# Optimization experiments

Hardware: AMD Instinct MI355X
Metric: run time of the kernel (lower is better)

## Reference

```python
import jax, jax.numpy as jnp
import numpy as np

B, T, H, W, C = 8, 32, 64, 64, 3
F = 24        # conv filters
U = 128       # lstm units
O = 1         # output units

def _conv(x, w, b):
    # x: [N,H,W,Cin], w: [3,3,Cin,Cout], SAME padding, linear activation
    y = jax.lax.conv_general_dilated(x, w, window_strides=(1, 1), padding='SAME',
                                     dimension_numbers=('NHWC', 'HWIO', 'NHWC'))
    return y + b

def setup_inputs() -> dict:
    key = jax.random.key(0)
    ks = jax.random.split(key, 16)
    s = lambda *shape: 0.05
    inp = {
        'x': jax.random.normal(ks[0], (B, T, H, W, C), dtype=jnp.float32),
        'conv1_w': jax.random.normal(ks[1], (3, 3, C, F), dtype=jnp.float32) * 0.1,
        'conv1_b': jnp.zeros((F,), jnp.float32),
        'conv2_w': jax.random.normal(ks[2], (3, 3, F, F), dtype=jnp.float32) * 0.1,
        'conv2_b': jnp.zeros((F,), jnp.float32),
        'Wf': jax.random.normal(ks[3], (F + U, U), dtype=jnp.float32) * 0.08,
        'bf': jnp.zeros((U,), jnp.float32),
        'Wi': jax.random.normal(ks[4], (F + U, U), dtype=jnp.float32) * 0.08,
        'bi': jnp.zeros((U,), jnp.float32),
        'Wc': jax.random.normal(ks[5], (F + U, U), dtype=jnp.float32) * 0.08,
        'bc': jnp.zeros((U,), jnp.float32),
        'Wo': jax.random.normal(ks[6], (F + U, U), dtype=jnp.float32) * 0.08,
        'bo': jnp.zeros((U,), jnp.float32),
        'out_w': jax.random.normal(ks[7], (U, O), dtype=jnp.float32) * 0.08,
        'out_b': jnp.zeros((O,), jnp.float32),
    }
    return inp

def reference(x, conv1_w, conv1_b, conv2_w, conv2_b, Wf, bf, Wi, bi, Wc, bc, Wo, bo, out_w, out_b):
    b, t, h, w, c = x.shape
    # CNN block (per-frame): two linear 3x3 convs, no pooling inside block
    xr = x.reshape(b * t, h, w, c)
    xr = _conv(xr, conv1_w, conv1_b)
    xr = _conv(xr, conv2_w, conv2_b)
    # TimeDistributed(GlobalAvgPool2D): mean over H,W -> [B,T,F]
    feat = xr.reshape(b, t, h, w, -1).mean(axis=(2, 3))

    # custom LSTM recurrence over time via scan
    def step(carry, xt):
        hs, cs = carry
        z = jnp.concatenate([xt, hs], axis=-1)           # [B, F+U]
        f = jax.nn.sigmoid(z @ Wf + bf)
        i = jax.nn.sigmoid(z @ Wi + bi)
        g = jnp.tanh(z @ Wc + bc)
        o = jax.nn.sigmoid(z @ Wo + bo)
        c_new = cs * f + i * g
        h_new = jnp.tanh(c_new) * o
        return (h_new, c_new), h_new

    h0 = jnp.zeros((b, Wf.shape[1]), x.dtype)
    c0 = jnp.zeros((b, Wf.shape[1]), x.dtype)
    _, hs = jax.lax.scan(step, (h0, c0), jnp.swapaxes(feat, 0, 1))  # [T,B,U]
    hs = jnp.swapaxes(hs, 0, 1)                                     # [B,T,U]
    return hs @ out_w + out_b                                       # [B,T,O]
```

## Files before the change

### kernel.cpp

```cpp
#include <hip/hip_runtime.h>
#include <math.h>

#define Bb 8
#define Tt 32
#define Hh 64
#define Ww 64
#define Cc 3
#define Ff 24
#define Uu 128

__global__ void convfeat_kernel(const float* __restrict__ x,
                                const float* __restrict__ w1, const float* __restrict__ b1,
                                const float* __restrict__ w2, const float* __restrict__ b2,
                                float* __restrict__ feat) {
    int n = blockIdx.x;
    const float* xf = x + (size_t)n * (Hh * Ww * Cc);
    int tid  = threadIdx.x;
    int row  = tid >> 2;
    int part = tid & 3;

    __shared__ float partial[256][3];
    __shared__ float rowsum[64][3];
    __shared__ float colv[64][12];
    __shared__ float st[75];
    __shared__ float yst[24][9];

    float s0 = 0.f, s1 = 0.f, s2 = 0.f;
    const float4* p4 = (const float4*)(xf + (row * Ww + part * 16) * Cc);
#pragma unroll
    for (int i = 0; i < 12; ++i) {
        float4 v = p4[i];
        int j = i * 4;
        float vv[4] = {v.x, v.y, v.z, v.w};
#pragma unroll
        for (int l = 0; l < 4; ++l) {
            int c = (j + l) % 3;
            if (c == 0) s0 += vv[l]; else if (c == 1) s1 += vv[l]; else s2 += vv[l];
        }
    }
    partial[tid][0] = s0; partial[tid][1] = s1; partial[tid][2] = s2;

    if (tid < 64) {
        int r = tid;
#pragma unroll
        for (int w4 = 0; w4 < 4; ++w4) {
            int w = (w4 < 2) ? w4 : 60 + w4;
#pragma unroll
            for (int c = 0; c < 3; ++c) colv[r][w4 * 3 + c] = xf[(r * Ww + w) * Cc + c];
        }
    }
    __syncthreads();

    if (part == 0) {
#pragma unroll
        for (int c = 0; c < 3; ++c)
            rowsum[row][c] = partial[tid][c] + partial[tid + 1][c]
                           + partial[tid + 2][c] + partial[tid + 3][c];
    }
    __syncthreads();

    if (tid < 3) {
        float t = 0.f;
        for (int r = 0; r < 64; ++r) t += rowsum[r][tid];
        st[tid * 25 + 0] = t;
    }
    if (tid >= 4 && tid < 16) {
        int k = tid - 4; int ri = k / 3, c = k % 3;
        int r = (ri < 2) ? ri : 60 + ri;
        st[c * 25 + 1 + ri] = rowsum[r][c];
    }
    if (tid >= 64 && tid < 76) {
        int k = tid - 64;
        float t = 0.f;
        for (int r = 0; r < 64; ++r) t += colv[r][k];
        int wi = k / 3, c = k % 3;
        st[c * 25 + 5 + wi] = t;
    }
    if (tid >= 128 && tid < 176) {
        int k = tid - 128; int pos = k / 3, c = k % 3;
        int ri = pos >> 2, wi = pos & 3;
        int r = (ri < 2) ? ri : 60 + ri;
        int w = (wi < 2) ? wi : 60 + wi;
        st[c * 25 + 9 + pos] = xf[(r * Ww + w) * Cc + c];
    }
    __syncthreads();

    if (tid < 24) {
        int f = tid;
        float Sy = 0, r0 = 0, r63 = 0, c0 = 0, c63 = 0, y00 = 0, y0W = 0, yH0 = 0, yHW = 0;
        for (int c = 0; c < 3; ++c) {
            const float* S = st + c * 25;
            float Sx = S[0];
            float rX[4] = {S[1], S[2], S[3], S[4]};
            float cX[4] = {S[5], S[6], S[7], S[8]};
            const float* X = S + 9;
            #define W1(p, q) w1[(((p) * 3 + (q)) * 3 + c) * 24 + f]
#pragma unroll
            for (int p = 0; p < 3; ++p)
#pragma unroll
                for (int q = 0; q < 3; ++q) {
                    float t = Sx;
                    if (p == 0) t -= rX[3];
                    if (p == 2) t -= rX[0];
                    if (q == 0) t -= cX[3];
                    if (q == 2) t -= cX[0];
                    if (p == 0 && q == 0) t += X[3 * 4 + 3];
                    if (p == 0 && q == 2) t += X[3 * 4 + 0];
                    if (p == 2 && q == 0) t += X[0 * 4 + 3];
                    if (p == 2 && q == 2) t += X[0 * 4 + 0];
                    Sy += W1(p, q) * t;
                }
#pragma unroll
            for (int q = 0; q < 3; ++q) {
                float Rr0  = rX[0] - ((q == 0) ? X[0 * 4 + 3] : 0.f) - ((q == 2) ? X[0 * 4 + 0] : 0.f);
                float Rr1  = rX[1] - ((q == 0) ? X[1 * 4 + 3] : 0.f) - ((q == 2) ? X[1 * 4 + 0] : 0.f);
                float Rr62 = rX[2] - ((q == 0) ? X[2 * 4 + 3] : 0.f) - ((q == 2) ? X[2 * 4 + 0] : 0.f);
                float Rr63 = rX[3] - ((q == 0) ? X[3 * 4 + 3] : 0.f) - ((q == 2) ? X[3 * 4 + 0] : 0.f);
                r0  += W1(1, q) * Rr0  + W1(2, q) * Rr1;
                r63 += W1(0, q) * Rr62 + W1(1, q) * Rr63;
            }
#pragma unroll
            for (int p = 0; p < 3; ++p) {
                float Rc0  = cX[0] - ((p == 0) ? X[3 * 4 + 0] : 0.f) - ((p == 2) ? X[0 * 4 + 0] : 0.f);
                float Rc1  = cX[1] - ((p == 0) ? X[3 * 4 + 1] : 0.f) - ((p == 2) ? X[0 * 4 + 1] : 0.f);
                float Rc62 = cX[2] - ((p == 0) ? X[3 * 4 + 2] : 0.f) - ((p == 2) ? X[0 * 4 + 2] : 0.f);
                float Rc63 = cX[3] - ((p == 0) ? X[3 * 4 + 3] : 0.f) - ((p == 2) ? X[0 * 4 + 3] : 0.f);
                c0  += W1(p, 1) * Rc0  + W1(p, 2) * Rc1;
                c63 += W1(p, 0) * Rc62 + W1(p, 1) * Rc63;
            }
            y00 += W1(1, 1) * X[0 * 4 + 0] + W1(1, 2) * X[0 * 4 + 1]
                 + W1(2, 1) * X[1 * 4 + 0] + W1(2, 2) * X[1 * 4 + 1];
            y0W += W1(1, 0) * X[0 * 4 + 2] + W1(1, 1) * X[0 * 4 + 3]
                 + W1(2, 0) * X[1 * 4 + 2] + W1(2, 1) * X[1 * 4 + 3];
            yH0 += W1(0, 1) * X[2 * 4 + 0] + W1(0, 2) * X[2 * 4 + 1]
                 + W1(1, 1) * X[3 * 4 + 0] + W1(1, 2) * X[3 * 4 + 1];
            yHW += W1(0, 0) * X[2 * 4 + 2] + W1(0, 1) * X[2 * 4 + 3]
                 + W1(1, 0) * X[3 * 4 + 2] + W1(1, 1) * X[3 * 4 + 3];
            #undef W1
        }
        float bb = b1[f];
        yst[f][0] = Sy + 4096.f * bb;
        yst[f][1] = r0 + 64.f * bb;
        yst[f][2] = r63 + 64.f * bb;
        yst[f][3] = c0 + 64.f * bb;
        yst[f][4] = c63 + 64.f * bb;
        yst[f][5] = y00 + bb; yst[f][6] = y0W + bb;
        yst[f][7] = yH0 + bb; yst[f][8] = yHW + bb;
    }
    __syncthreads();

    if (tid < 24) {
        int g = tid;
        float acc = 0.f;
        for (int f = 0; f < 24; ++f) {
            float Sy = yst[f][0], rY0 = yst[f][1], rY63 = yst[f][2], cY0 = yst[f][3], cY63 = yst[f][4];
            float yc00 = yst[f][5], yc0W = yst[f][6], ycH0 = yst[f][7], ycHW = yst[f][8];
#pragma unroll
            for (int p = 0; p < 3; ++p)
#pragma unroll
                for (int q = 0; q < 3; ++q) {
                    float t = Sy;
                    if (p == 0) t -= rY63;
                    if (p == 2) t -= rY0;
                    if (q == 0) t -= cY63;
                    if (q == 2) t -= cY0;
                    if (p == 0 && q == 0) t += ycHW;
                    if (p == 0 && q == 2) t += ycH0;
                    if (p == 2 && q == 0) t += yc0W;
                    if (p == 2 && q == 2) t += yc00;
                    acc += w2[(((p * 3 + q) * 24 + f) * 24) + g] * t;
                }
        }
        feat[(size_t)n * 24 + g] = b2[g] + acc * (1.f / 4096.f);
    }
}

__global__ void gpre_kernel(const float* __restrict__ feat,
                            const float* __restrict__ Wf, const float* __restrict__ bf,
                            const float* __restrict__ Wi, const float* __restrict__ bi,
                            const float* __restrict__ Wc, const float* __restrict__ bc,
                            const float* __restrict__ Wo, const float* __restrict__ bo,
                            float* __restrict__ G) {
    int blk = blockIdx.x;
    int t = blk >> 3, b = blk & 7;
    int tid = threadIdx.x;
    int g = tid >> 7, u = tid & 127;
    const float* W    = (g == 0) ? Wf : (g == 1) ? Wi : (g == 2) ? Wc : Wo;
    const float* bias = (g == 0) ? bf : (g == 1) ? bi : (g == 2) ? bc : bo;
    int n = b * Tt + t;
    float acc = bias[u];
#pragma unroll
    for (int k = 0; k < Ff; ++k) acc += feat[(size_t)n * Ff + k] * W[k * Uu + u];
    G[(size_t)blk * 512 + tid] = acc;
}

__global__ __launch_bounds__(512, 1) void lstm_kernel(
        const float* __restrict__ G,
        const float* __restrict__ Wf, const float* __restrict__ Wi,
        const float* __restrict__ Wc, const float* __restrict__ Wo,
        const float* __restrict__ out_w, const float* __restrict__ out_b,
        float* __restrict__ out) {
    int b = blockIdx.x;
    int tid = threadIdx.x;
    int u = tid & 127;
    int q = tid >> 7;

    float wreg[32][4];
    {
        const float* W0 = Wf + (size_t)(Ff + q * 32) * Uu + u;
        const float* W1 = Wi + (size_t)(Ff + q * 32) * Uu + u;
        const float* W2 = Wc + (size_t)(Ff + q * 32) * Uu + u;
        const float* W3 = Wo + (size_t)(Ff + q * 32) * Uu + u;
#pragma unroll
        for (int j = 0; j < 32; ++j) {
            wreg[j][0] = W0[j * Uu];
            wreg[j][1] = W1[j * Uu];
            wreg[j][2] = W2[j * Uu];
            wreg[j][3] = W3[j * Uu];
        }
    }

    __shared__ float hs[Uu];
    __shared__ float part[4][4][Uu];
    __shared__ float act[4][Uu];
    __shared__ float hist[Tt][Uu];

    float cs = 0.f;
    if (tid < Uu) hs[tid] = 0.f;
    __syncthreads();

    for (int t = 0; t < Tt; ++t) {
        float gx = G[((size_t)(t * Bb + b)) * 512 + tid];

        float p0 = 0.f, p1 = 0.f, p2 = 0.f, p3 = 0.f;
        const float4* h4 = (const float4*)(hs + q * 32);
#pragma unroll
        for (int j4 = 0; j4 < 8; ++j4) {
            float4 hv = h4[j4];
            p0 += wreg[j4 * 4 + 0][0] * hv.x; p1 += wreg[j4 * 4 + 0][1] * hv.x;
            p2 += wreg[j4 * 4 + 0][2] * hv.x; p3 += wreg[j4 * 4 + 0][3] * hv.x;
            p0 += wreg[j4 * 4 + 1][0] * hv.y; p1 += wreg[j4 * 4 + 1][1] * hv.y;
            p2 += wreg[j4 * 4 + 1][2] * hv.y; p3 += wreg[j4 * 4 + 1][3] * hv.y;
            p0 += wreg[j4 * 4 + 2][0] * hv.z; p1 += wreg[j4 * 4 + 2][1] * hv.z;
            p2 += wreg[j4 * 4 + 2][2] * hv.z; p3 += wreg[j4 * 4 + 2][3] * hv.z;
            p0 += wreg[j4 * 4 + 3][0] * hv.w; p1 += wreg[j4 * 4 + 3][1] * hv.w;
            p2 += wreg[j4 * 4 + 3][2] * hv.w; p3 += wreg[j4 * 4 + 3][3] * hv.w;
        }
        part[q][0][u] = p0; part[q][1][u] = p1;
        part[q][2][u] = p2; part[q][3][u] = p3;
        __syncthreads();

        float s = part[0][q][u] + part[1][q][u] + part[2][q][u] + part[3][q][u] + gx;
        float a = (q == 2) ? tanhf(s) : 1.f / (1.f + expf(-s));
        act[q][u] = a;
        __syncthreads();

        if (tid < Uu) {
            float f = act[0][u], i = act[1][u], g = act[2][u], o = act[3][u];
            cs = cs * f + i * g;
            float hn = tanhf(cs) * o;
            hs[u] = hn;
            hist[t][u] = hn;
        }
        __syncthreads();
    }

    int tt = tid >> 4, j = tid & 15;
    const float4* hh = (const float4*)(&hist[tt][j * 8]);
    float4 a0 = hh[0], a1 = hh[1];
    const float* owp = out_w + j * 8;
    float pw = a0.x * owp[0] + a0.y * owp[1] + a0.z * owp[2] + a0.w * owp[3]
             + a1.x * owp[4] + a1.y * owp[5] + a1.z * owp[6] + a1.w * owp[7];
#pragma unroll
    for (int off = 8; off > 0; off >>= 1) pw += __shfl_down(pw, off, 16);
    if (j == 0) out[b * Tt + tt] = pw + out_b[0];
}

extern "C" void kernel_launch(void* const* d_in, const int* in_sizes, int n_in,
                              void* d_out, int out_size, void* d_ws, size_t ws_size,
                              hipStream_t stream) {
    const float* x   = (const float*)d_in[0];
    const float* w1  = (const float*)d_in[1];
    const float* b1  = (const float*)d_in[2];
    const float* w2  = (const float*)d_in[3];
    const float* b2  = (const float*)d_in[4];
    const float* Wf  = (const float*)d_in[5];
    const float* bf  = (const float*)d_in[6];
    const float* Wi  = (const float*)d_in[7];
    const float* bi  = (const float*)d_in[8];
    const float* Wc  = (const float*)d_in[9];
    const float* bc  = (const float*)d_in[10];
    const float* Wo  = (const float*)d_in[11];
    const float* bo  = (const float*)d_in[12];
    const float* ow  = (const float*)d_in[13];
    const float* ob  = (const float*)d_in[14];
    float* out = (float*)d_out;

    float* ws   = (float*)d_ws;
    float* feat = ws;
    float* G    = ws + 6144;

    convfeat_kernel<<<Bb * Tt, 256, 0, stream>>>(x, w1, b1, w2, b2, feat);
    gpre_kernel<<<Bb * Tt, 512, 0, stream>>>(feat, Wf, bf, Wi, bi, Wc, bc, Wo, bo, G);
    lstm_kernel<<<Bb, 512, 0, stream>>>(G, Wf, Wi, Wc, Wo, ow, ob, out);
}
```

Baseline: 42.96 us.

## Fuse input-gate projection into LSTM kernel and use packed FMA with fast activations

Removes the separate gpre kernel launch and its workspace round trip by computing each thread's 24-term input projection inside the LSTM time loop. Each thread now holds the recurrent weights for two units across two gates, so the matmul can use v_pk_fma_f32 inline assembly. Gate partials go to a 16-row shared buffer, and one barrier per step is dropped by doing the activations in the reduction threads. tanh and sigmoid switch to exp2/rcp approximations, which add a little numerical error and leave the activation work serialized in 128 threads.

New measurement: 50.16 us. +16.8%, slower.

```diff
diff --git a/kernel.cpp b/kernel.cpp
--- a/kernel.cpp
+++ b/kernel.cpp
@@ -8,6 +8,17 @@
 #define Cc 3
 #define Ff 24
 #define Uu 128
+
+typedef float v2f __attribute__((ext_vector_type(2)));
+
+__device__ __forceinline__ float fast_sigmoid(float x) {
+    float e = __builtin_amdgcn_exp2f(-1.442695040888963f * x);
+    return __builtin_amdgcn_rcpf(1.f + e);
+}
+__device__ __forceinline__ float fast_tanh(float x) {
+    float e = __builtin_amdgcn_exp2f(-2.885390081777927f * x);
+    return 2.f * __builtin_amdgcn_rcpf(1.f + e) - 1.f;
+}
 
 __global__ void convfeat_kernel(const float* __restrict__ x,
                                 const float* __restrict__ w1, const float* __restrict__ b1,
@@ -175,90 +186,89 @@
     }
 }
 
-__global__ void gpre_kernel(const float* __restrict__ feat,
-                            const float* __restrict__ Wf, const float* __restrict__ bf,
-                            const float* __restrict__ Wi, const float* __restrict__ bi,
-                            const float* __restrict__ Wc, const float* __restrict__ bc,
-                            const float* __restrict__ Wo, const float* __restrict__ bo,
-                            float* __restrict__ G) {
-    int blk = blockIdx.x;
-    int t = blk >> 3, b = blk & 7;
-    int tid = threadIdx.x;
-    int g = tid >> 7, u = tid & 127;
-    const float* W    = (g == 0) ? Wf : (g == 1) ? Wi : (g == 2) ? Wc : Wo;
-    const float* bias = (g == 0) ? bf : (g == 1) ? bi : (g == 2) ? bc : bo;
-    int n = b * Tt + t;
-    float acc = bias[u];
-#pragma unroll
-    for (int k = 0; k < Ff; ++k) acc += feat[(size_t)n * Ff + k] * W[k * Uu + u];
-    G[(size_t)blk * 512 + tid] = acc;
-}
-
 __global__ __launch_bounds__(512, 1) void lstm_kernel(
-        const float* __restrict__ G,
-        const float* __restrict__ Wf, const float* __restrict__ Wi,
-        const float* __restrict__ Wc, const float* __restrict__ Wo,
+        const float* __restrict__ feat,
+        const float* __restrict__ Wf, const float* __restrict__ bf,
+        const float* __restrict__ Wi, const float* __restrict__ bi,
+        const float* __restrict__ Wc, const float* __restrict__ bc,
+        const float* __restrict__ Wo, const float* __restrict__ bo,
         const float* __restrict__ out_w, const float* __restrict__ out_b,
         float* __restrict__ out) {
-    int b = blockIdx.x;
+    int b   = blockIdx.x;
     int tid = threadIdx.x;
-    int u = tid & 127;
-    int q = tid >> 7;
-
-    float wreg[32][4];
-    {
-        const float* W0 = Wf + (size_t)(Ff + q * 32) * Uu + u;
-        const float* W1 = Wi + (size_t)(Ff + q * 32) * Uu + u;
-        const float* W2 = Wc + (size_t)(Ff + q * 32) * Uu + u;
-        const float* W3 = Wo + (size_t)(Ff + q * 32) * Uu + u;
-#pragma unroll
-        for (int j = 0; j < 32; ++j) {
-            wreg[j][0] = W0[j * Uu];
-            wreg[j][1] = W1[j * Uu];
-            wreg[j][2] = W2[j * Uu];
-            wreg[j][3] = W3[j * Uu];
-        }
-    }
+    int up  = tid & 63;
+    int q   = (tid >> 6) & 3;
+    int s   = tid >> 8;
+
+    const float* Wg0 = (s == 0) ? Wf : Wc;
+    const float* Wg1 = (s == 0) ? Wi : Wo;
+
+    v2f w0[32], w1[32];
+#pragma unroll
+    for (int r = 0; r < 32; ++r) {
+        w0[r] = *(const v2f*)(Wg0 + (size_t)(Ff + 32 * q + r) * Uu + 2 * up);
+        w1[r] = *(const v2f*)(Wg1 + (size_t)(Ff + 32 * q + r) * Uu + 2 * up);
+    }
+
+    const float* Wgx = (q & 1) ? Wg1 : Wg0;
+    const float* bgx = (s == 0) ? ((q & 1) ? bi : bf) : ((q & 1) ? bo : bc);
+    int ucol = 2 * up + ((q >> 1) & 1);
+    float w24[Ff];
+#pragma unroll
+    for (int k = 0; k < Ff; ++k) w24[k] = Wgx[(size_t)k * Uu + ucol];
+    float biasv = bgx[ucol];
 
     __shared__ float hs[Uu];
-    __shared__ float part[4][4][Uu];
-    __shared__ float act[4][Uu];
+    __shared__ float part[16][Uu];
     __shared__ float hist[Tt][Uu];
 
     float cs = 0.f;
     if (tid < Uu) hs[tid] = 0.f;
     __syncthreads();
 
+    const float* ftb = feat + (size_t)(b * Tt) * Ff;
+
     for (int t = 0; t < Tt; ++t) {
-        float gx = G[((size_t)(t * Bb + b)) * 512 + tid];
-
-        float p0 = 0.f, p1 = 0.f, p2 = 0.f, p3 = 0.f;
-        const float4* h4 = (const float4*)(hs + q * 32);
-#pragma unroll
-        for (int j4 = 0; j4 < 8; ++j4) {
-            float4 hv = h4[j4];
-            p0 += wreg[j4 * 4 + 0][0] * hv.x; p1 += wreg[j4 * 4 + 0][1] * hv.x;
-            p2 += wreg[j4 * 4 + 0][2] * hv.x; p3 += wreg[j4 * 4 + 0][3] * hv.x;
-            p0 += wreg[j4 * 4 + 1][0] * hv.y; p1 += wreg[j4 * 4 + 1][1] * hv.y;
-            p2 += wreg[j4 * 4 + 1][2] * hv.y; p3 += wreg[j4 * 4 + 1][3] * hv.y;
-            p0 += wreg[j4 * 4 + 2][0] * hv.z; p1 += wreg[j4 * 4 + 2][1] * hv.z;
-            p2 += wreg[j4 * 4 + 2][2] * hv.z; p3 += wreg[j4 * 4 + 2][3] * hv.z;
-            p0 += wreg[j4 * 4 + 3][0] * hv.w; p1 += wreg[j4 * 4 + 3][1] * hv.w;
-            p2 += wreg[j4 * 4 + 3][2] * hv.w; p3 += wreg[j4 * 4 + 3][3] * hv.w;
-        }
-        part[q][0][u] = p0; part[q][1][u] = p1;
-        part[q][2][u] = p2; part[q][3][u] = p3;
+        float gxv = biasv;
+        const float* ft = ftb + t * Ff;
+#pragma unroll
+        for (int k = 0; k < Ff; ++k) gxv = fmaf(ft[k], w24[k], gxv);
+
+        v2f acc0 = {0.f, 0.f}, acc1 = {0.f, 0.f};
+        const v2f* hp = (const v2f*)(hs + q * 32);
+#pragma unroll
+        for (int j = 0; j < 16; ++j) {
+            v2f h2 = hp[j];
+            asm("v_pk_fma_f32 %0, %2, %3, %0 op_sel:[0,0,0] op_sel_hi:[1,0,1]\n\t"
+                "v_pk_fma_f32 %1, %4, %3, %1 op_sel:[0,0,0] op_sel_hi:[1,0,1]"
+                : "+v"(acc0), "+v"(acc1)
+                : "v"(w0[2 * j]), "v"(h2), "v"(w1[2 * j]));
+            asm("v_pk_fma_f32 %0, %2, %3, %0 op_sel:[0,1,0] op_sel_hi:[1,1,1]\n\t"
+                "v_pk_fma_f32 %1, %4, %3, %1 op_sel:[0,1,0] op_sel_hi:[1,1,1]"
+                : "+v"(acc0), "+v"(acc1)
+                : "v"(w0[2 * j + 1]), "v"(h2), "v"(w1[2 * j + 1]));
+        }
+
+        if ((q & 1) == 0) { if (q & 2) acc0.y += gxv; else acc0.x += gxv; }
+        else              { if (q & 2) acc1.y += gxv; else acc1.x += gxv; }
+
+        v2f* pb = (v2f*)part;
+        pb[(q * 4 + 2 * s + 0) * 64 + up] = acc0;
+        pb[(q * 4 + 2 * s + 1) * 64 + up] = acc1;
         __syncthreads();
 
-        float s = part[0][q][u] + part[1][q][u] + part[2][q][u] + part[3][q][u] + gx;
-        float a = (q == 2) ? tanhf(s) : 1.f / (1.f + expf(-s));
-        act[q][u] = a;
-        __syncthreads();
-
         if (tid < Uu) {
-            float f = act[0][u], i = act[1][u], g = act[2][u], o = act[3][u];
+            int u = tid;
+            float sf = part[0][u]  + part[4][u]  + part[8][u]  + part[12][u];
+            float si = part[1][u]  + part[5][u]  + part[9][u]  + part[13][u];
+            float sg = part[2][u]  + part[6][u]  + part[10][u] + part[14][u];
+            float so = part[3][u]  + part[7][u]  + part[11][u] + part[15][u];
+            float f = fast_sigmoid(sf);
+            float i = fast_sigmoid(si);
+            float g = fast_tanh(sg);
+            float o = fast_sigmoid(so);
             cs = cs * f + i * g;
-            float hn = tanhf(cs) * o;
+            float hn = fast_tanh(cs) * o;
             hs[u] = hn;
             hist[t][u] = hn;
         }
@@ -296,11 +306,9 @@
     const float* ob  = (const float*)d_in[14];
     float* out = (float*)d_out;
 
-    float* ws   = (float*)d_ws;
-    float* feat = ws;
-    float* G    = ws + 6144;
+    float* feat = (float*)d_ws;
 
     convfeat_kernel<<<Bb * Tt, 256, 0, stream>>>(x, w1, b1, w2, b2, feat);
-    gpre_kernel<<<Bb * Tt, 512, 0, stream>>>(feat, Wf, bf, Wi, bi, Wc, bc, Wo, bo, G);
-    lstm_kernel<<<Bb, 512, 0, stream>>>(G, Wf, Wi, Wc, Wo, ow, ob, out);
-}
+    lstm_kernel<<<Bb, 512, 0, stream>>>(feat, Wf, bf, Wi, bi, Wc, bc, Wo, bo,
+                                        ow, ob, out);
+}
```

## Restructure LSTM recurrence to 1024 threads with packed FMA and fast activations

Applied to the files above, without the earlier changes.

The LSTM kernel now uses 1024 threads per batch element. Each thread holds 32 rows by 2 columns of one gate's recurrent weights and accumulates with v_pk_fma_f32 inline asm. Activations are folded into the final per-unit stage, using exp2/rcp intrinsics instead of expf/tanhf, which removes one barrier per timestep. The trade-offs are a lower-precision fast tanh/sigmoid and the serial per-unit gate work being concentrated in 128 threads.

Result: slower. 45.49 us (+5.9%).

```diff
diff --git a/kernel.cpp b/kernel.cpp
--- a/kernel.cpp
+++ b/kernel.cpp
@@ -8,6 +8,17 @@
 #define Cc 3
 #define Ff 24
 #define Uu 128
+
+typedef float v2f __attribute__((ext_vector_type(2)));
+
+__device__ __forceinline__ float fast_sigmoid(float x) {
+    float e = __builtin_amdgcn_exp2f(-1.442695040888963f * x);
+    return __builtin_amdgcn_rcpf(1.f + e);
+}
+__device__ __forceinline__ float fast_tanh(float x) {
+    float e = __builtin_amdgcn_exp2f(-2.885390081777927f * x);
+    return 2.f * __builtin_amdgcn_rcpf(1.f + e) - 1.f;
+}
 
 __global__ void convfeat_kernel(const float* __restrict__ x,
                                 const float* __restrict__ w1, const float* __restrict__ b1,
@@ -194,35 +205,26 @@
     G[(size_t)blk * 512 + tid] = acc;
 }
 
-__global__ __launch_bounds__(512, 1) void lstm_kernel(
+__global__ __launch_bounds__(1024, 1) void lstm_kernel(
         const float* __restrict__ G,
         const float* __restrict__ Wf, const float* __restrict__ Wi,
         const float* __restrict__ Wc, const float* __restrict__ Wo,
         const float* __restrict__ out_w, const float* __restrict__ out_b,
         float* __restrict__ out) {
-    int b = blockIdx.x;
+    int b   = blockIdx.x;
     int tid = threadIdx.x;
-    int u = tid & 127;
-    int q = tid >> 7;
-
-    float wreg[32][4];
-    {
-        const float* W0 = Wf + (size_t)(Ff + q * 32) * Uu + u;
-        const float* W1 = Wi + (size_t)(Ff + q * 32) * Uu + u;
-        const float* W2 = Wc + (size_t)(Ff + q * 32) * Uu + u;
-        const float* W3 = Wo + (size_t)(Ff + q * 32) * Uu + u;
-#pragma unroll
-        for (int j = 0; j < 32; ++j) {
-            wreg[j][0] = W0[j * Uu];
-            wreg[j][1] = W1[j * Uu];
-            wreg[j][2] = W2[j * Uu];
-            wreg[j][3] = W3[j * Uu];
-        }
-    }
+    int up  = tid & 63;
+    int g   = (tid >> 6) & 3;
+    int q   = tid >> 8;
+    const float* Wg = (g == 0) ? Wf : (g == 1) ? Wi : (g == 2) ? Wc : Wo;
+
+    v2f w[32];
+#pragma unroll
+    for (int r = 0; r < 32; ++r)
+        w[r] = *(const v2f*)(Wg + (size_t)(Ff + 32 * q + r) * Uu + 2 * up);
 
     __shared__ float hs[Uu];
-    __shared__ float part[4][4][Uu];
-    __shared__ float act[4][Uu];
+    __shared__ float part[16][Uu];
     __shared__ float hist[Tt][Uu];
 
     float cs = 0.f;
@@ -230,49 +232,51 @@
     __syncthreads();
 
     for (int t = 0; t < Tt; ++t) {
-        float gx = G[((size_t)(t * Bb + b)) * 512 + tid];
-
-        float p0 = 0.f, p1 = 0.f, p2 = 0.f, p3 = 0.f;
-        const float4* h4 = (const float4*)(hs + q * 32);
-#pragma unroll
-        for (int j4 = 0; j4 < 8; ++j4) {
-            float4 hv = h4[j4];
-            p0 += wreg[j4 * 4 + 0][0] * hv.x; p1 += wreg[j4 * 4 + 0][1] * hv.x;
-            p2 += wreg[j4 * 4 + 0][2] * hv.x; p3 += wreg[j4 * 4 + 0][3] * hv.x;
-            p0 += wreg[j4 * 4 + 1][0] * hv.y; p1 += wreg[j4 * 4 + 1][1] * hv.y;
-            p2 += wreg[j4 * 4 + 1][2] * hv.y; p3 += wreg[j4 * 4 + 1][3] * hv.y;
-            p0 += wreg[j4 * 4 + 2][0] * hv.z; p1 += wreg[j4 * 4 + 2][1] * hv.z;
-            p2 += wreg[j4 * 4 + 2][2] * hv.z; p3 += wreg[j4 * 4 + 2][3] * hv.z;
-            p0 += wreg[j4 * 4 + 3][0] * hv.w; p1 += wreg[j4 * 4 + 3][1] * hv.w;
-            p2 += wreg[j4 * 4 + 3][2] * hv.w; p3 += wreg[j4 * 4 + 3][3] * hv.w;
-        }
-        part[q][0][u] = p0; part[q][1][u] = p1;
-        part[q][2][u] = p2; part[q][3][u] = p3;
+        float g0 = 0.f, g1 = 0.f, g2 = 0.f, g3 = 0.f;
+        if (tid < Uu) {
+            const float* Gt = G + ((size_t)(t * Bb + b)) * 512 + tid;
+            g0 = Gt[0]; g1 = Gt[128]; g2 = Gt[256]; g3 = Gt[384];
+        }
+
+        v2f ae = {0.f, 0.f}, ao = {0.f, 0.f};
+        const v2f* hp = (const v2f*)(hs + q * 32);
+#pragma unroll
+        for (int j = 0; j < 16; ++j) {
+            v2f h2 = hp[j];
+            asm("v_pk_fma_f32 %0, %1, %2, %0 op_sel:[0,0,0] op_sel_hi:[1,0,1]"
+                : "+v"(ae) : "v"(w[2 * j]), "v"(h2));
+            asm("v_pk_fma_f32 %0, %1, %2, %0 op_sel:[0,1,0] op_sel_hi:[1,1,1]"
+                : "+v"(ao) : "v"(w[2 * j + 1]), "v"(h2));
+        }
+        v2f acc = ae + ao;
+        *(v2f*)&part[q * 4 + g][2 * up] = acc;
         __syncthreads();
 
-        float s = part[0][q][u] + part[1][q][u] + part[2][q][u] + part[3][q][u] + gx;
-        float a = (q == 2) ? tanhf(s) : 1.f / (1.f + expf(-s));
-        act[q][u] = a;
-        __syncthreads();
-
         if (tid < Uu) {
-            float f = act[0][u], i = act[1][u], g = act[2][u], o = act[3][u];
-            cs = cs * f + i * g;
-            float hn = tanhf(cs) * o;
+            int u = tid;
+            float sf = part[0][u] + part[4][u] + part[8][u]  + part[12][u] + g0;
+            float si = part[1][u] + part[5][u] + part[9][u]  + part[13][u] + g1;
+            float sg = part[2][u] + part[6][u] + part[10][u] + part[14][u] + g2;
+            float so = part[3][u] + part[7][u] + part[11][u] + part[15][u] + g3;
+            float f  = fast_sigmoid(sf);
+            float i  = fast_sigmoid(si);
+            float gg = fast_tanh(sg);
+            float o  = fast_sigmoid(so);
+            cs = cs * f + i * gg;
+            float hn = fast_tanh(cs) * o;
             hs[u] = hn;
             hist[t][u] = hn;
         }
         __syncthreads();
     }
 
-    int tt = tid >> 4, j = tid & 15;
-    const float4* hh = (const float4*)(&hist[tt][j * 8]);
-    float4 a0 = hh[0], a1 = hh[1];
-    const float* owp = out_w + j * 8;
-    float pw = a0.x * owp[0] + a0.y * owp[1] + a0.z * owp[2] + a0.w * owp[3]
-             + a1.x * owp[4] + a1.y * owp[5] + a1.z * owp[6] + a1.w * owp[7];
-#pragma unroll
-    for (int off = 8; off > 0; off >>= 1) pw += __shfl_down(pw, off, 16);
+    int tt = tid >> 5, j = tid & 31;
+    const float4* hh = (const float4*)(&hist[tt][j * 4]);
+    float4 a0 = hh[0];
+    const float* owp = out_w + j * 4;
+    float pw = a0.x * owp[0] + a0.y * owp[1] + a0.z * owp[2] + a0.w * owp[3];
+#pragma unroll
+    for (int off = 16; off > 0; off >>= 1) pw += __shfl_down(pw, off, 32);
     if (j == 0) out[b * Tt + tt] = pw + out_b[0];
 }
 
@@ -302,5 +306,5 @@
 
     convfeat_kernel<<<Bb * Tt, 256, 0, stream>>>(x, w1, b1, w2, b2, feat);
     gpre_kernel<<<Bb * Tt, 512, 0, stream>>>(feat, Wf, bf, Wi, bi, Wc, bc, Wo, bo, G);
-    lstm_kernel<<<Bb, 512, 0, stream>>>(G, Wf, Wi, Wc, Wo, ow, ob, out);
-}
+    lstm_kernel<<<Bb, 1024, 0, stream>>>(G, Wf, Wi, Wc, Wo, ow, ob, out);
+}
```
